# Optimization experiments

Measured on AMD Instinct MI355X. Metric: run time of the kernel, lower is better.

The kernel has to match this reference:

```python
import jax, jax.numpy as jnp
import numpy as np

DIM = 1024
DIM_HEAD = 64
HEADS = DIM // DIM_HEAD  # 16
WINDOW = 128
EPS = 1e-5


def rotate_half(x):
    # rearrange '(r d) -> r d' with r=2: first half is x1, second half is x2
    d = x.shape[-1] // 2
    x1, x2 = x[..., :d], x[..., d:]
    return jnp.concatenate((-x2, x1), axis=-1)


def setup_inputs() -> dict:
    key = jax.random.key(0)
    k0, k1, k2 = jax.random.split(key, 3)
    B, T = 4, 8192
    x = jax.random.normal(k0, (B, DIM, T), dtype=jnp.float32)
    ln_w = jnp.ones((DIM,), jnp.float32)
    ln_b = jnp.zeros((DIM,), jnp.float32)
    w_qkv = jax.random.normal(k1, (3 * DIM, DIM), jnp.float32) * (DIM ** -0.5)
    w_out = jax.random.normal(k2, (DIM, DIM), jnp.float32) * (DIM ** -0.5)
    return {"x": x, "ln_w": ln_w, "ln_b": ln_b, "w_qkv": w_qkv, "w_out": w_out}


def reference(x, ln_w, ln_b, w_qkv, w_out):
    B, C, T = x.shape
    residual = x
    h = x.transpose(0, 2, 1)  # (B, T, C)
    # LayerNorm over channel dim (eqx default eps=1e-5)
    mu = h.mean(-1, keepdims=True)
    var = ((h - mu) ** 2).mean(-1, keepdims=True)
    h = (h - mu) / jnp.sqrt(var + EPS) * ln_w + ln_b
    # QKV projection (eqx Linear: y = W @ x -> x @ W.T)
    qkv = h @ w_qkv.T  # (B, T, 3C)
    q, k, v = jnp.split(qkv, 3, axis=-1)
    w = T // WINDOW
    def to_heads(t):
        # 'b (w n) (h d) -> b h w n d'
        return t.reshape(B, w, WINDOW, HEADS, DIM_HEAD).transpose(0, 3, 1, 2, 4)
    q, k, v = map(to_heads, (q, k, v))  # (B, H, w, n, d)
    # Rotary embeddings over the window axis (seq_len = WINDOW), xpos disabled -> scale = 1
    inv_freq = 1.0 / 10000 ** (jnp.arange(0, DIM_HEAD, 2, dtype=jnp.float32) / DIM_HEAD)
    t_pos = jnp.arange(WINDOW, dtype=jnp.float32)
    freqs = jnp.einsum('i,j->ij', t_pos, inv_freq)
    freqs = jnp.concatenate((freqs, freqs), axis=-1)  # (n, d)
    cos, sin = jnp.cos(freqs), jnp.sin(freqs)
    q = q * cos + rotate_half(q) * sin
    k = k * cos + rotate_half(k) * sin
    # Windowed scaled dot-product attention (no mask)
    scores = jnp.einsum('bhwnd,bhwmd->bhwnm', q, k) / jnp.sqrt(jnp.float32(DIM_HEAD))
    attn = jax.nn.softmax(scores, axis=-1)
    out = jnp.einsum('bhwnm,bhwmd->bhwnd', attn, v)
    # 'b h w n d -> b (w n) (h d)'
    out = out.transpose(0, 2, 3, 1, 4).reshape(B, T, C)
    out = out @ w_out.T
    return out.transpose(0, 2, 1) + residual
```

## Files before the change

### kernel.cpp

```cpp
#include <hip/hip_runtime.h>
#include <hip/hip_bf16.h>

#define DIMC 1024
#define DH   64
#define NH   16
#define WIN  128
#define TT   8192
#define BB   4
#define NTOK 32768
#define NQKV 3072

typedef __hip_bfloat16 bf16;
typedef __attribute__((ext_vector_type(8))) __bf16 b16x8;
typedef __attribute__((ext_vector_type(4))) float  f32x4;

__device__ __forceinline__ void gload_lds16(const void* g, void* l) {
  __builtin_amdgcn_global_load_lds((__attribute__((address_space(1))) void*)g,
                                   (__attribute__((address_space(3))) void*)l,
                                   16, 0, 0);
}

__global__ void k_stats_partial(const float* __restrict__ x,
                                float* __restrict__ psum, float* __restrict__ psq) {
  int g = blockIdx.x * 256 + threadIdx.x;
  int s = blockIdx.y;
  int b = g >> 13;
  int t = g & (TT - 1);
  const float* xp = x + ((size_t)b * DIMC + s * 128) * TT + t;
  float sum = 0.f, sq = 0.f;
  for (int c = 0; c < 128; c++) {
    float v = xp[(size_t)c * TT];
    sum += v; sq += v * v;
  }
  psum[s * NTOK + g] = sum;
  psq [s * NTOK + g] = sq;
}

__global__ void k_stats_final(const float* __restrict__ psum, const float* __restrict__ psq,
                              float* __restrict__ mean, float* __restrict__ rstd) {
  int g = blockIdx.x * 256 + threadIdx.x;
  float s = 0.f, q = 0.f;
  for (int i = 0; i < 8; i++) { s += psum[i * NTOK + g]; q += psq[i * NTOK + g]; }
  float mu = s * (1.0f / 1024.0f);
  float var = q * (1.0f / 1024.0f) - mu * mu;
  mean[g] = mu;
  rstd[g] = rsqrtf(var + 1e-5f);
}

__global__ void k_norm_t(const float* __restrict__ x, const float* __restrict__ mean,
                         const float* __restrict__ rstd, const float* __restrict__ lnw,
                         const float* __restrict__ lnb, bf16* __restrict__ h) {
  __shared__ float tile[32][33];
  int b = blockIdx.z, c0 = blockIdx.y * 32, t0 = blockIdx.x * 32;
  int col = threadIdx.x & 31, rr = threadIdx.x >> 5;
  for (int i = 0; i < 4; i++) {
    int c = rr + i * 8;
    tile[c][col] = x[((size_t)b * DIMC + c0 + c) * TT + t0 + col];
  }
  __syncthreads();
  for (int i = 0; i < 4; i++) {
    int t = rr + i * 8;
    int g = b * TT + t0 + t;
    float mu = mean[g], rs = rstd[g];
    float v = (tile[col][t] - mu) * rs * lnw[c0 + col] + lnb[c0 + col];
    h[((size_t)(b * TT + t0 + t)) * DIMC + c0 + col] = __float2bfloat16(v);
  }
}

__global__ void k_cast(const float* __restrict__ wqkv, const float* __restrict__ wout,
                       bf16* __restrict__ wqkvb, bf16* __restrict__ woutb) {
  size_t i = (size_t)blockIdx.x * 256 + threadIdx.x;
  if (i < (size_t)NQKV * DIMC) wqkvb[i] = __float2bfloat16(wqkv[i]);
  if (i < (size_t)DIMC * DIMC) woutb[i] = __float2bfloat16(wout[i]);
}

__global__ __launch_bounds__(256) void k_gemm_bt(const bf16* __restrict__ A,
                                                 const bf16* __restrict__ Bm,
                                                 bf16* __restrict__ C,
                                                 int M, int N, int K) {
  __shared__ __align__(16) bf16 As[128 * 32];
  __shared__ __align__(16) bf16 Bs[128 * 32];
  int tid = threadIdx.x;
  int wave = tid >> 6, lane = tid & 63;
  int m0 = blockIdx.y * 128, n0 = blockIdx.x * 128;
  int wm = (wave >> 1) * 64, wn = (wave & 1) * 64;
  int lr = lane & 15, quad = lane >> 4;
  int srow = lane >> 2;
  int scol = (lane & 3) * 8;

  f32x4 acc[4][4];
#pragma unroll
  for (int i = 0; i < 4; i++)
#pragma unroll
    for (int j = 0; j < 4; j++) acc[i][j] = (f32x4){0.f, 0.f, 0.f, 0.f};

  for (int k0 = 0; k0 < K; k0 += 32) {
#pragma unroll
    for (int r = 0; r < 2; r++) {
      int chunk = r * 4 + wave;
      int row = chunk * 16 + srow;
      gload_lds16(A  + (size_t)(m0 + row) * K + k0 + scol, As + row * 32 + scol);
      gload_lds16(Bm + (size_t)(n0 + row) * K + k0 + scol, Bs + row * 32 + scol);
    }
    __syncthreads();
    b16x8 af[4], bfr[4];
#pragma unroll
    for (int i = 0; i < 4; i++) af[i]  = *(const b16x8*)(As + (wm + i * 16 + lr) * 32 + quad * 8);
#pragma unroll
    for (int j = 0; j < 4; j++) bfr[j] = *(const b16x8*)(Bs + (wn + j * 16 + lr) * 32 + quad * 8);
#pragma unroll
    for (int i = 0; i < 4; i++)
#pragma unroll
      for (int j = 0; j < 4; j++)
        acc[i][j] = __builtin_amdgcn_mfma_f32_16x16x32_bf16(af[i], bfr[j], acc[i][j], 0, 0, 0);
    __syncthreads();
  }

#pragma unroll
  for (int i = 0; i < 4; i++)
#pragma unroll
    for (int j = 0; j < 4; j++) {
      int row = m0 + wm + i * 16 + quad * 4;
      int col = n0 + wn + j * 16 + lr;
      bf16* cp = C + (size_t)row * N + col;
#pragma unroll
      for (int r = 0; r < 4; r++) cp[(size_t)r * N] = __float2bfloat16(acc[i][j][r]);
    }
}

__global__ __launch_bounds__(256) void k_attn(const bf16* __restrict__ qkv,
                                              bf16* __restrict__ att) {
  __shared__ __align__(16) char smem[54272];
  bf16* qs = (bf16*)smem;
  bf16* ks = (bf16*)(smem + 18432);
  bf16* vt = (bf16*)(smem + 36864);
  bf16* ps = (bf16*)smem;

  const int tid = threadIdx.x;
  const int wdw = blockIdx.x, hh = blockIdx.y, b = blockIdx.z;
  const size_t base = ((size_t)(b * TT + wdw * WIN)) * NQKV + hh * DH;

  for (int idx = tid; idx < 128 * 32; idx += 256) {
    int row = idx >> 5, j = idx & 31;
    float invf = exp2f(-0.41524101186f * (float)j);
    float fr = (float)row * invf;
    float sv, cv;
    __sincosf(fr, &sv, &cv);
    const bf16* qp = qkv + base + (size_t)row * NQKV;
    float q0 = __bfloat162float(qp[j]);
    float q1 = __bfloat162float(qp[j + 32]);
    qs[row * 72 + j]      = __float2bfloat16(q0 * cv - q1 * sv);
    qs[row * 72 + j + 32] = __float2bfloat16(q1 * cv + q0 * sv);
    float ka = __bfloat162float(qp[1024 + j]);
    float kb = __bfloat162float(qp[1024 + j + 32]);
    ks[row * 72 + j]      = __float2bfloat16(ka * cv - kb * sv);
    ks[row * 72 + j + 32] = __float2bfloat16(kb * cv + ka * sv);
  }
  for (int idx = tid; idx < 128 * 64; idx += 256) {
    int row = idx >> 6, d = idx & 63;
    vt[d * 136 + row] = qkv[base + (size_t)row * NQKV + 2048 + d];
  }
  __syncthreads();

  const int wid = tid >> 6, lane = tid & 63;
  const int lr = lane & 15, quad = lane >> 4;

  f32x4 sa[2][8];
#pragma unroll
  for (int i = 0; i < 2; i++)
#pragma unroll
    for (int nt = 0; nt < 8; nt++) sa[i][nt] = (f32x4){0.f, 0.f, 0.f, 0.f};

  b16x8 aq[2][2];
#pragma unroll
  for (int i = 0; i < 2; i++)
#pragma unroll
    for (int s = 0; s < 2; s++)
      aq[i][s] = *(const b16x8*)(qs + (wid * 32 + i * 16 + lr) * 72 + s * 32 + quad * 8);
#pragma unroll
  for (int nt = 0; nt < 8; nt++) {
    b16x8 b0 = *(const b16x8*)(ks + (nt * 16 + lr) * 72 + quad * 8);
    b16x8 b1 = *(const b16x8*)(ks + (nt * 16 + lr) * 72 + 32 + quad * 8);
#pragma unroll
    for (int i = 0; i < 2; i++) {
      sa[i][nt] = __builtin_amdgcn_mfma_f32_16x16x32_bf16(aq[i][0], b0, sa[i][nt], 0, 0, 0);
      sa[i][nt] = __builtin_amdgcn_mfma_f32_16x16x32_bf16(aq[i][1], b1, sa[i][nt], 0, 0, 0);
    }
  }
  __syncthreads();

#pragma unroll
  for (int i = 0; i < 2; i++) {
#pragma unroll
    for (int r = 0; r < 4; r++) {
      float vals[8];
      float mx = -1e30f;
#pragma unroll
      for (int nt = 0; nt < 8; nt++) { vals[nt] = sa[i][nt][r] * 0.125f; mx = fmaxf(mx, vals[nt]); }
      for (int m = 1; m < 16; m <<= 1) mx = fmaxf(mx, __shfl_xor(mx, m, 16));
      float sum = 0.f;
#pragma unroll
      for (int nt = 0; nt < 8; nt++) { vals[nt] = __expf(vals[nt] - mx); sum += vals[nt]; }
      for (int m = 1; m < 16; m <<= 1) sum += __shfl_xor(sum, m, 16);
      float inv = 1.0f / sum;
      int row = wid * 32 + i * 16 + quad * 4 + r;
#pragma unroll
      for (int nt = 0; nt < 8; nt++)
        ps[row * 136 + nt * 16 + lr] = __float2bfloat16(vals[nt] * inv);
    }
  }
  __syncthreads();

  f32x4 oa[2][4];
#pragma unroll
  for (int i = 0; i < 2; i++)
#pragma unroll
    for (int nt = 0; nt < 4; nt++) oa[i][nt] = (f32x4){0.f, 0.f, 0.f, 0.f};
#pragma unroll
  for (int s = 0; s < 4; s++) {
    b16x8 ap[2];
#pragma unroll
    for (int i = 0; i < 2; i++)
      ap[i] = *(const b16x8*)(ps + (wid * 32 + i * 16 + lr) * 136 + s * 32 + quad * 8);
#pragma unroll
    for (int nt = 0; nt < 4; nt++) {
      b16x8 bv = *(const b16x8*)(vt + (nt * 16 + lr) * 136 + s * 32 + quad * 8);
#pragma unroll
      for (int i = 0; i < 2; i++)
        oa[i][nt] = __builtin_amdgcn_mfma_f32_16x16x32_bf16(ap[i], bv, oa[i][nt], 0, 0, 0);
    }
  }
#pragma unroll
  for (int i = 0; i < 2; i++)
#pragma unroll
    for (int nt = 0; nt < 4; nt++) {
      int row = wid * 32 + i * 16 + quad * 4;
#pragma unroll
      for (int r = 0; r < 4; r++)
        att[((size_t)(b * TT + wdw * WIN + row + r)) * DIMC + hh * DH + nt * 16 + lr] =
            __float2bfloat16(oa[i][nt][r]);
    }
}

__global__ void k_out_res(const bf16* __restrict__ g, const float* __restrict__ x,
                          float* __restrict__ out) {
  __shared__ float tile[32][33];
  int b = blockIdx.z, c0 = blockIdx.y * 32, t0 = blockIdx.x * 32;
  int col = threadIdx.x & 31, rr = threadIdx.x >> 5;
  for (int i = 0; i < 4; i++) {
    int t = rr + i * 8;
    tile[t][col] = __bfloat162float(g[((size_t)(b * TT + t0 + t)) * DIMC + c0 + col]);
  }
  __syncthreads();
  for (int i = 0; i < 4; i++) {
    int c = rr + i * 8;
    size_t o = ((size_t)b * DIMC + c0 + c) * TT + t0 + col;
    out[o] = x[o] + tile[col][c];
  }
}

extern "C" void kernel_launch(void* const* d_in, const int* in_sizes, int n_in,
                              void* d_out, int out_size, void* d_ws, size_t ws_size,
                              hipStream_t stream) {
  const float* x    = (const float*)d_in[0];
  const float* lnw  = (const float*)d_in[1];
  const float* lnb  = (const float*)d_in[2];
  const float* wqkv = (const float*)d_in[3];
  const float* wout = (const float*)d_in[4];
  float* out = (float*)d_out;

  char* ws = (char*)d_ws;
  float* psum  = (float*)(ws);
  float* psq   = (float*)(ws + (size_t)1  * 1024 * 1024);
  float* meanp = (float*)(ws + (size_t)2  * 1024 * 1024);
  float* rstdp = (float*)(ws + (size_t)2  * 1024 * 1024 + 131072);
  bf16*  wqkvb = (bf16*) (ws + (size_t)4  * 1024 * 1024);
  bf16*  woutb = (bf16*) (ws + (size_t)10 * 1024 * 1024);
  bf16*  h     = (bf16*) (ws + (size_t)12 * 1024 * 1024);
  bf16*  qkv   = (bf16*) (ws + (size_t)76 * 1024 * 1024);
  bf16*  att   = h;
  bf16*  g2    = qkv;

  k_stats_partial<<<dim3(NTOK / 256, 8), 256, 0, stream>>>(x, psum, psq);
  k_stats_final<<<dim3(NTOK / 256), 256, 0, stream>>>(psum, psq, meanp, rstdp);
  k_norm_t<<<dim3(TT / 32, DIMC / 32, BB), 256, 0, stream>>>(x, meanp, rstdp, lnw, lnb, h);
  k_cast<<<dim3((NQKV * DIMC) / 256), 256, 0, stream>>>(wqkv, wout, wqkvb, woutb);
  k_gemm_bt<<<dim3(NQKV / 128, NTOK / 128), 256, 0, stream>>>(h, wqkvb, qkv, NTOK, NQKV, DIMC);
  k_attn<<<dim3(TT / WIN, NH, BB), 256, 0, stream>>>(qkv, att);
  k_gemm_bt<<<dim3(DIMC / 128, NTOK / 128), 256, 0, stream>>>(att, woutb, g2, NTOK, DIMC, DIMC);
  k_out_res<<<dim3(TT / 32, DIMC / 32, BB), 256, 0, stream>>>(g2, x, out);
}
```

Measured before the change: 841.3 us.

## Vectorize LN kernels, swizzle GEMM LDS with K=64 tiles, fuse residual into out-proj

The stats and final kernels now load float4 vectors. The normalize-transpose kernel uses 64x64 tiles and writes 16-byte bf16 stores. The GEMM K-step grows from 32 to 64 with an XOR-swizzled LDS layout to avoid bank conflicts, and its epilogue is staged through LDS for coalesced 16-byte stores. The output projection gets its own kernel that writes its result transposed and adds the residual directly, which removes the intermediate bf16 buffer and the separate transpose-add pass. Risks are added LDS traffic and extra syncs in the epilogues, plus higher register pressure from the larger K step.

```diff
diff --git a/kernel.cpp b/kernel.cpp
--- a/kernel.cpp
+++ b/kernel.cpp
@@ -14,6 +14,8 @@
 typedef __attribute__((ext_vector_type(8))) __bf16 b16x8;
 typedef __attribute__((ext_vector_type(4))) float  f32x4;
 
+union BV { b16x8 v; bf16 h[8]; };
+
 __device__ __forceinline__ void gload_lds16(const void* g, void* l) {
   __builtin_amdgcn_global_load_lds((__attribute__((address_space(1))) void*)g,
                                    (__attribute__((address_space(3))) void*)l,
@@ -22,48 +24,68 @@
 
 __global__ void k_stats_partial(const float* __restrict__ x,
                                 float* __restrict__ psum, float* __restrict__ psq) {
-  int g = blockIdx.x * 256 + threadIdx.x;
+  int g4 = blockIdx.x * 256 + threadIdx.x;
   int s = blockIdx.y;
-  int b = g >> 13;
-  int t = g & (TT - 1);
+  int t4 = g4 * 4;
+  int b = t4 >> 13;
+  int t = t4 & (TT - 1);
   const float* xp = x + ((size_t)b * DIMC + s * 128) * TT + t;
-  float sum = 0.f, sq = 0.f;
+  float4 sum = {0.f, 0.f, 0.f, 0.f}, sq = {0.f, 0.f, 0.f, 0.f};
   for (int c = 0; c < 128; c++) {
-    float v = xp[(size_t)c * TT];
-    sum += v; sq += v * v;
-  }
-  psum[s * NTOK + g] = sum;
-  psq [s * NTOK + g] = sq;
+    float4 v = *(const float4*)(xp + (size_t)c * TT);
+    sum.x += v.x; sum.y += v.y; sum.z += v.z; sum.w += v.w;
+    sq.x += v.x * v.x; sq.y += v.y * v.y; sq.z += v.z * v.z; sq.w += v.w * v.w;
+  }
+  *(float4*)(psum + s * NTOK + t4) = sum;
+  *(float4*)(psq  + s * NTOK + t4) = sq;
 }
 
 __global__ void k_stats_final(const float* __restrict__ psum, const float* __restrict__ psq,
                               float* __restrict__ mean, float* __restrict__ rstd) {
-  int g = blockIdx.x * 256 + threadIdx.x;
-  float s = 0.f, q = 0.f;
-  for (int i = 0; i < 8; i++) { s += psum[i * NTOK + g]; q += psq[i * NTOK + g]; }
-  float mu = s * (1.0f / 1024.0f);
-  float var = q * (1.0f / 1024.0f) - mu * mu;
-  mean[g] = mu;
-  rstd[g] = rsqrtf(var + 1e-5f);
-}
-
-__global__ void k_norm_t(const float* __restrict__ x, const float* __restrict__ mean,
-                         const float* __restrict__ rstd, const float* __restrict__ lnw,
-                         const float* __restrict__ lnb, bf16* __restrict__ h) {
-  __shared__ float tile[32][33];
-  int b = blockIdx.z, c0 = blockIdx.y * 32, t0 = blockIdx.x * 32;
-  int col = threadIdx.x & 31, rr = threadIdx.x >> 5;
-  for (int i = 0; i < 4; i++) {
-    int c = rr + i * 8;
-    tile[c][col] = x[((size_t)b * DIMC + c0 + c) * TT + t0 + col];
-  }
-  __syncthreads();
-  for (int i = 0; i < 4; i++) {
-    int t = rr + i * 8;
+  int g4 = (blockIdx.x * 256 + threadIdx.x) * 4;
+  float4 s = {0.f, 0.f, 0.f, 0.f}, q = {0.f, 0.f, 0.f, 0.f};
+  for (int i = 0; i < 8; i++) {
+    float4 a = *(const float4*)(psum + i * NTOK + g4);
+    float4 bq = *(const float4*)(psq + i * NTOK + g4);
+    s.x += a.x; s.y += a.y; s.z += a.z; s.w += a.w;
+    q.x += bq.x; q.y += bq.y; q.z += bq.z; q.w += bq.w;
+  }
+  float4 mu = {s.x * (1.f/1024.f), s.y * (1.f/1024.f), s.z * (1.f/1024.f), s.w * (1.f/1024.f)};
+  float4 rs;
+  rs.x = rsqrtf(q.x * (1.f/1024.f) - mu.x * mu.x + 1e-5f);
+  rs.y = rsqrtf(q.y * (1.f/1024.f) - mu.y * mu.y + 1e-5f);
+  rs.z = rsqrtf(q.z * (1.f/1024.f) - mu.z * mu.z + 1e-5f);
+  rs.w = rsqrtf(q.w * (1.f/1024.f) - mu.w * mu.w + 1e-5f);
+  *(float4*)(mean + g4) = mu;
+  *(float4*)(rstd + g4) = rs;
+}
+
+__global__ __launch_bounds__(256) void k_norm_t(const float* __restrict__ x,
+                         const float* __restrict__ mean, const float* __restrict__ rstd,
+                         const float* __restrict__ lnw, const float* __restrict__ lnb,
+                         bf16* __restrict__ h) {
+  __shared__ float tile[64][65];
+  int b = blockIdx.z, c0 = blockIdx.y * 64, t0 = blockIdx.x * 64;
+  int tid = threadIdx.x;
+  int tq = (tid & 15) * 4;
+  for (int ci = 0; ci < 4; ci++) {
+    int c = ci * 16 + (tid >> 4);
+    float4 v = *(const float4*)&x[((size_t)b * DIMC + c0 + c) * TT + t0 + tq];
+    tile[c][tq] = v.x; tile[c][tq + 1] = v.y; tile[c][tq + 2] = v.z; tile[c][tq + 3] = v.w;
+  }
+  __syncthreads();
+  for (int it = 0; it < 2; it++) {
+    int t = it * 32 + (tid >> 3);
+    int cg = tid & 7;
     int g = b * TT + t0 + t;
     float mu = mean[g], rs = rstd[g];
-    float v = (tile[col][t] - mu) * rs * lnw[c0 + col] + lnb[c0 + col];
-    h[((size_t)(b * TT + t0 + t)) * DIMC + c0 + col] = __float2bfloat16(v);
+    BV u;
+    for (int k = 0; k < 8; k++) {
+      int c = cg * 8 + k;
+      float v = (tile[c][t] - mu) * rs * lnw[c0 + c] + lnb[c0 + c];
+      u.h[k] = __float2bfloat16(v);
+    }
+    *(b16x8*)(h + (size_t)g * DIMC + c0 + cg * 8) = u.v;
   }
 }
 
@@ -74,19 +96,55 @@
   if (i < (size_t)DIMC * DIMC) woutb[i] = __float2bfloat16(wout[i]);
 }
 
+#define GEMM_KLOOP(A_, B_, K_)                                                   \
+  for (int k0 = 0; k0 < (K_); k0 += 64) {                                        \
+    _Pragma("unroll")                                                            \
+    for (int r = 0; r < 4; r++) {                                                \
+      int chunk = r * 4 + wave;                                                  \
+      int row = chunk * 8 + srow;                                                \
+      gload_lds16((A_) + (size_t)(m0 + row) * (K_) + k0 + scol,                  \
+                  As + chunk * 512 + lane * 8);                                  \
+      gload_lds16((B_) + (size_t)(n0 + row) * (K_) + k0 + scol,                  \
+                  Bs + chunk * 512 + lane * 8);                                  \
+    }                                                                            \
+    __syncthreads();                                                             \
+    _Pragma("unroll")                                                            \
+    for (int s = 0; s < 2; s++) {                                                \
+      b16x8 af[4], bfr[4];                                                       \
+      _Pragma("unroll")                                                          \
+      for (int i = 0; i < 4; i++) {                                              \
+        int row = wm + i * 16 + lr;                                              \
+        af[i] = *(const b16x8*)(As + row * 64 + ((((s << 2) + quad) ^ (row & 7)) << 3)); \
+      }                                                                          \
+      _Pragma("unroll")                                                          \
+      for (int j = 0; j < 4; j++) {                                              \
+        int row = wn + j * 16 + lr;                                              \
+        bfr[j] = *(const b16x8*)(Bs + row * 64 + ((((s << 2) + quad) ^ (row & 7)) << 3)); \
+      }                                                                          \
+      _Pragma("unroll")                                                          \
+      for (int i = 0; i < 4; i++)                                                \
+        _Pragma("unroll")                                                        \
+        for (int j = 0; j < 4; j++)                                              \
+          acc[i][j] = __builtin_amdgcn_mfma_f32_16x16x32_bf16(af[i], bfr[j], acc[i][j], 0, 0, 0); \
+    }                                                                            \
+    __syncthreads();                                                             \
+  }
+
 __global__ __launch_bounds__(256) void k_gemm_bt(const bf16* __restrict__ A,
                                                  const bf16* __restrict__ Bm,
                                                  bf16* __restrict__ C,
                                                  int M, int N, int K) {
-  __shared__ __align__(16) bf16 As[128 * 32];
-  __shared__ __align__(16) bf16 Bs[128 * 32];
+  __shared__ __align__(16) char smem[32768];
+  bf16* As = (bf16*)smem;
+  bf16* Bs = (bf16*)(smem + 16384);
+  bf16* Cs = (bf16*)smem;
   int tid = threadIdx.x;
   int wave = tid >> 6, lane = tid & 63;
   int m0 = blockIdx.y * 128, n0 = blockIdx.x * 128;
   int wm = (wave >> 1) * 64, wn = (wave & 1) * 64;
   int lr = lane & 15, quad = lane >> 4;
-  int srow = lane >> 2;
-  int scol = (lane & 3) * 8;
+  int srow = lane >> 3;
+  int scol = ((lane & 7) ^ srow) * 8;
 
   f32x4 acc[4][4];
 #pragma unroll
@@ -94,38 +152,74 @@
 #pragma unroll
     for (int j = 0; j < 4; j++) acc[i][j] = (f32x4){0.f, 0.f, 0.f, 0.f};
 
-  for (int k0 = 0; k0 < K; k0 += 32) {
-#pragma unroll
-    for (int r = 0; r < 2; r++) {
-      int chunk = r * 4 + wave;
-      int row = chunk * 16 + srow;
-      gload_lds16(A  + (size_t)(m0 + row) * K + k0 + scol, As + row * 32 + scol);
-      gload_lds16(Bm + (size_t)(n0 + row) * K + k0 + scol, Bs + row * 32 + scol);
-    }
+  GEMM_KLOOP(A, Bm, K)
+
+#pragma unroll
+  for (int i = 0; i < 4; i++)
+#pragma unroll
+    for (int j = 0; j < 4; j++)
+#pragma unroll
+      for (int r = 0; r < 4; r++)
+        Cs[(wm + i * 16 + quad * 4 + r) * 128 + wn + j * 16 + lr] =
+            __float2bfloat16(acc[i][j][r]);
+  __syncthreads();
+#pragma unroll
+  for (int it = 0; it < 8; it++) {
+    int row = it * 16 + (tid >> 4), cg = tid & 15;
+    *(b16x8*)(C + (size_t)(m0 + row) * N + n0 + cg * 8) = *(b16x8*)(Cs + row * 128 + cg * 8);
+  }
+}
+
+__global__ __launch_bounds__(256) void k_gemm_out(const bf16* __restrict__ A,
+                                                  const bf16* __restrict__ Bm,
+                                                  const float* __restrict__ x,
+                                                  float* __restrict__ out) {
+  const int K = DIMC, N = DIMC;
+  __shared__ __align__(16) char smem[32768];
+  bf16* As = (bf16*)smem;
+  bf16* Bs = (bf16*)(smem + 16384);
+  float* ls = (float*)smem;
+  int tid = threadIdx.x;
+  int wave = tid >> 6, lane = tid & 63;
+  int m0 = blockIdx.y * 128, n0 = blockIdx.x * 128;
+  int wm = (wave >> 1) * 64, wn = (wave & 1) * 64;
+  int lr = lane & 15, quad = lane >> 4;
+  int srow = lane >> 3;
+  int scol = ((lane & 7) ^ srow) * 8;
+
+  f32x4 acc[4][4];
+#pragma unroll
+  for (int i = 0; i < 4; i++)
+#pragma unroll
+    for (int j = 0; j < 4; j++) acc[i][j] = (f32x4){0.f, 0.f, 0.f, 0.f};
+
+  GEMM_KLOOP(A, Bm, K)
+
+  int b = m0 >> 13, t0 = m0 & (TT - 1);
+  int tl = tid & 31, cc = tid >> 5;
+  for (int ch = 0; ch < 4; ch++) {
     __syncthreads();
-    b16x8 af[4], bfr[4];
-#pragma unroll
-    for (int i = 0; i < 4; i++) af[i]  = *(const b16x8*)(As + (wm + i * 16 + lr) * 32 + quad * 8);
-#pragma unroll
-    for (int j = 0; j < 4; j++) bfr[j] = *(const b16x8*)(Bs + (wn + j * 16 + lr) * 32 + quad * 8);
-#pragma unroll
-    for (int i = 0; i < 4; i++)
-#pragma unroll
-      for (int j = 0; j < 4; j++)
-        acc[i][j] = __builtin_amdgcn_mfma_f32_16x16x32_bf16(af[i], bfr[j], acc[i][j], 0, 0, 0);
+    if ((ch >> 1) == (wave & 1)) {
+      int jb = (ch & 1) * 2;
+#pragma unroll
+      for (int jj = 0; jj < 2; jj++)
+#pragma unroll
+        for (int i = 0; i < 4; i++)
+#pragma unroll
+          for (int r = 0; r < 4; r++)
+            ls[(jj * 16 + lr) * 140 + wm + i * 16 + quad * 4 + r] = acc[i][jb + jj][r];
+    }
     __syncthreads();
-  }
-
-#pragma unroll
-  for (int i = 0; i < 4; i++)
-#pragma unroll
-    for (int j = 0; j < 4; j++) {
-      int row = m0 + wm + i * 16 + quad * 4;
-      int col = n0 + wn + j * 16 + lr;
-      bf16* cp = C + (size_t)row * N + col;
-#pragma unroll
-      for (int r = 0; r < 4; r++) cp[(size_t)r * N] = __float2bfloat16(acc[i][j][r]);
-    }
+#pragma unroll
+    for (int cit = 0; cit < 4; cit++) {
+      int c = cit * 8 + cc;
+      float4 v = *(float4*)(ls + c * 140 + tl * 4);
+      size_t o = ((size_t)(b * DIMC + n0 + ch * 32 + c)) * TT + t0 + tl * 4;
+      float4 xr = *(const float4*)(x + o);
+      v.x += xr.x; v.y += xr.y; v.z += xr.z; v.w += xr.w;
+      *(float4*)(out + o) = v;
+    }
+  }
 }
 
 __global__ __launch_bounds__(256) void k_attn(const bf16* __restrict__ qkv,
@@ -242,23 +336,6 @@
     }
 }
 
-__global__ void k_out_res(const bf16* __restrict__ g, const float* __restrict__ x,
-                          float* __restrict__ out) {
-  __shared__ float tile[32][33];
-  int b = blockIdx.z, c0 = blockIdx.y * 32, t0 = blockIdx.x * 32;
-  int col = threadIdx.x & 31, rr = threadIdx.x >> 5;
-  for (int i = 0; i < 4; i++) {
-    int t = rr + i * 8;
-    tile[t][col] = __bfloat162float(g[((size_t)(b * TT + t0 + t)) * DIMC + c0 + col]);
-  }
-  __syncthreads();
-  for (int i = 0; i < 4; i++) {
-    int c = rr + i * 8;
-    size_t o = ((size_t)b * DIMC + c0 + c) * TT + t0 + col;
-    out[o] = x[o] + tile[col][c];
-  }
-}
-
 extern "C" void kernel_launch(void* const* d_in, const int* in_sizes, int n_in,
                               void* d_out, int out_size, void* d_ws, size_t ws_size,
                               hipStream_t stream) {
@@ -279,14 +356,12 @@
   bf16*  h     = (bf16*) (ws + (size_t)12 * 1024 * 1024);
   bf16*  qkv   = (bf16*) (ws + (size_t)76 * 1024 * 1024);
   bf16*  att   = h;
-  bf16*  g2    = qkv;
-
-  k_stats_partial<<<dim3(NTOK / 256, 8), 256, 0, stream>>>(x, psum, psq);
-  k_stats_final<<<dim3(NTOK / 256), 256, 0, stream>>>(psum, psq, meanp, rstdp);
-  k_norm_t<<<dim3(TT / 32, DIMC / 32, BB), 256, 0, stream>>>(x, meanp, rstdp, lnw, lnb, h);
+
+  k_stats_partial<<<dim3(NTOK / 1024, 8), 256, 0, stream>>>(x, psum, psq);
+  k_stats_final<<<dim3(NTOK / 1024), 256, 0, stream>>>(psum, psq, meanp, rstdp);
+  k_norm_t<<<dim3(TT / 64, DIMC / 64, BB), 256, 0, stream>>>(x, meanp, rstdp, lnw, lnb, h);
   k_cast<<<dim3((NQKV * DIMC) / 256), 256, 0, stream>>>(wqkv, wout, wqkvb, woutb);
   k_gemm_bt<<<dim3(NQKV / 128, NTOK / 128), 256, 0, stream>>>(h, wqkvb, qkv, NTOK, NQKV, DIMC);
   k_attn<<<dim3(TT / WIN, NH, BB), 256, 0, stream>>>(qkv, att);
-  k_gemm_bt<<<dim3(DIMC / 128, NTOK / 128), 256, 0, stream>>>(att, woutb, g2, NTOK, DIMC, DIMC);
-  k_out_res<<<dim3(TT / 32, DIMC / 32, BB), 256, 0, stream>>>(g2, x, out);
-}
+  k_gemm_out<<<dim3(DIMC / 128, NTOK / 128), 256, 0, stream>>>(att, woutb, x, out);
+}
```

Measured after the change: 752.8 us. 1.12x faster.
